# Kernel tuning notes

Hardware: AMD Instinct MI355X
Metric: run time of the kernel (lower is better)

Reference implementation:

```python
import jax, jax.numpy as jnp
import numpy as np

N = 100000   # num_nodes
E = 1600000  # num_edges
H = 128      # hidden_dim
OUT = 1      # output_dim
SLOPE = 0.2  # GATConv leaky_relu negative_slope


def setup_inputs() -> dict:
    key = jax.random.key(0)
    ks = jax.random.split(key, 10)
    s = 1.0 / np.sqrt(H)
    return {
        "h": jnp.arange(N, dtype=jnp.int64 if jax.config.jax_enable_x64 else jnp.int32),
        "edge_index": jax.random.randint(ks[0], (2, E), 0, N),
        "node_type": jax.random.randint(ks[1], (N,), 0, 3),
        "emb": jax.random.normal(ks[2], (N, H), jnp.float32) * s,
        "W1": jax.random.normal(ks[3], (H, H), jnp.float32) * s,
        "a_src1": jax.random.normal(ks[4], (H,), jnp.float32) * s,
        "a_dst1": jax.random.normal(ks[5], (H,), jnp.float32) * s,
        "b1": jnp.zeros((H,), jnp.float32),
        "W2": jax.random.normal(ks[6], (H, OUT), jnp.float32) * s,
        "a_src2": jax.random.normal(ks[7], (OUT,), jnp.float32) * s,
        "a_dst2": jax.random.normal(ks[8], (OUT,), jnp.float32) * s,
        "b2": jnp.zeros((OUT,), jnp.float32),
    }


def gat_layer(x, src, dst, emask, W, a_src, a_dst, b, n_nodes):
    """PyG GATConv (heads=1, add_self_loops=True). Masked edges get -inf logits."""
    xp = x @ W                                  # [N, F]
    e_src = xp @ a_src                          # [N]
    e_dst = xp @ a_dst                          # [N]
    logits = jax.nn.leaky_relu(e_src[src] + e_dst[dst], SLOPE)   # [E]
    logits = jnp.where(emask, logits, -jnp.inf)
    self_logits = jax.nn.leaky_relu(e_src + e_dst, SLOPE)        # [N] self-loops
    # segment softmax over destination nodes (edges + self loop)
    m = jax.ops.segment_max(logits, dst, num_segments=n_nodes)
    m = jnp.maximum(m, self_logits)             # finite: self loop always present
    ew = jnp.exp(logits - m[dst])               # masked edges -> exp(-inf)=0
    sw = jnp.exp(self_logits - m)
    denom = jax.ops.segment_sum(ew, dst, num_segments=n_nodes) + sw
    alpha = ew / denom[dst]                     # [E]
    alpha_self = sw / denom                     # [N]
    out = jax.ops.segment_sum(alpha[:, None] * xp[src], dst, num_segments=n_nodes)
    out = out + alpha_self[:, None] * xp + b
    return out


def reference(h, edge_index, node_type, emb, W1, a_src1, a_dst1, b1, W2, a_src2, a_dst2, b2):
    src, dst = edge_index[0], edge_index[1]
    emask = (node_type[src] == 0) & (node_type[dst] == 0)
    x = emb[h]                                          # embedding lookup [N, H]
    x = gat_layer(x, src, dst, emask, W1, a_src1, a_dst1, b1, emb.shape[0])
    x = jax.nn.relu(x)
    x = gat_layer(x, src, dst, emask, W2, a_src2, a_dst2, b2, emb.shape[0])
    return x
```

## Files before the change

kernel.cpp:

```cpp
#include <hip/hip_runtime.h>

#define N_NODES 100000
#define N_EDGES 1600000
#define HD 128
#define SLOPE 0.2f
#define NBLK 391
#define EBLK (N_EDGES / 256)

typedef __attribute__((ext_vector_type(8))) short bf16x8;
typedef __attribute__((ext_vector_type(4))) float f32x4;

__device__ __forceinline__ unsigned short f2bf(float f) {
    union { float f; unsigned u; } v; v.f = f;
    const unsigned u = v.u + 0x7FFFu + ((v.u >> 16) & 1u);
    return (unsigned short)(u >> 16);
}
__device__ __forceinline__ unsigned pack2(float lo, float hi) {
    return (unsigned)f2bf(lo) | ((unsigned)f2bf(hi) << 16);
}
__device__ __forceinline__ float bf2f(unsigned u16) {
    union { unsigned u; float f; } v; v.u = u16 << 16; return v.f;
}

__global__ __launch_bounds__(256) void zero_kernel(
    const int* __restrict__ nt, const float* __restrict__ W1,
    int* __restrict__ deg, int* __restrict__ fill, unsigned* __restrict__ umask,
    unsigned short* __restrict__ W1bfT)
{
    const int i = blockIdx.x * 256 + threadIdx.x;
    bool act = false;
    if (i < N_NODES) { deg[i] = 0; fill[i] = 0; act = (nt[i] == 0); }
    const unsigned long long bal = __ballot(act);
    const int lane = threadIdx.x & 63;
    if (lane == 0)       umask[i >> 5] = (unsigned)bal;
    else if (lane == 32) umask[i >> 5] = (unsigned)(bal >> 32);
    if (i < HD * HD) {
        const int n = i >> 7, k = i & 127;
        W1bfT[n * HD + k] = f2bf(W1[k * HD + n]);
    }
}

__global__ __launch_bounds__(512, 8) void gemm1_kernel(
    const int* __restrict__ h,
    const float* __restrict__ emb,
    const unsigned short* __restrict__ W1bfT,
    const float* __restrict__ a_src1,
    const float* __restrict__ a_dst1,
    unsigned short* __restrict__ xp1,
    float* __restrict__ es1,
    float* __restrict__ ed1,
    float* __restrict__ denom1)
{
    __shared__ unsigned short Wlds[HD * HD];

    const int tid = threadIdx.x;

    {
        const int n  = tid >> 2;
        const int kq = (tid & 3) * 32;
        const unsigned short* src = W1bfT + n * HD + kq;
        #pragma unroll
        for (int j = 0; j < 4; ++j) {
            const int c = (kq >> 3) + j;
            const int p = c ^ (n & 7);
            *(bf16x8*)(Wlds + n * HD + p * 8) = *(const bf16x8*)(src + j * 8);
        }
    }

    const int w   = tid >> 6;
    const int L   = tid & 63;
    const int lm  = L & 15;
    const int lg  = L >> 4;
    const int wrow0 = blockIdx.x * 128 + w * 16;

    const int arow = wrow0 + lm;
    const int g = (arow < N_NODES) ? arow : (N_NODES - 1);
    const float* xrow = emb + (size_t)h[g] * HD;

    __syncthreads();

    f32x4 acc[8];
    #pragma unroll
    for (int ct = 0; ct < 8; ++ct) acc[ct] = (f32x4)0.f;

    #pragma unroll
    for (int ks = 0; ks < 4; ++ks) {
        const int k0 = ks * 32 + lg * 8;
        const float4 u = *(const float4*)(xrow + k0);
        const float4 v = *(const float4*)(xrow + k0 + 4);
        union { bf16x8 b; unsigned x[4]; } t;
        t.x[0] = pack2(u.x, u.y);
        t.x[1] = pack2(u.z, u.w);
        t.x[2] = pack2(v.x, v.y);
        t.x[3] = pack2(v.z, v.w);
        const bf16x8 af = t.b;

        const int c = k0 >> 3;
        const int p = (c ^ (lm & 7)) * 8;
        #pragma unroll
        for (int ct = 0; ct < 8; ++ct) {
            const bf16x8 bfr = *(const bf16x8*)(Wlds + (ct * 16 + lm) * HD + p);
            acc[ct] = __builtin_amdgcn_mfma_f32_16x16x32_bf16(af, bfr, acc[ct], 0, 0, 0);
        }
    }

    float asv[8], adv[8];
    #pragma unroll
    for (int ct = 0; ct < 8; ++ct) {
        asv[ct] = a_src1[ct * 16 + lm];
        adv[ct] = a_dst1[ct * 16 + lm];
    }

    #pragma unroll
    for (int reg = 0; reg < 4; ++reg) {
        const int row = wrow0 + lg * 4 + reg;
        float s = 0.f, d = 0.f;
        #pragma unroll
        for (int ct = 0; ct < 8; ++ct) {
            s += acc[ct][reg] * asv[ct];
            d += acc[ct][reg] * adv[ct];
        }
        #pragma unroll
        for (int m = 1; m < 16; m <<= 1) {
            s += __shfl_xor(s, m, 64);
            d += __shfl_xor(d, m, 64);
        }
        if (row < N_NODES) {
            unsigned short* dst = xp1 + (size_t)row * HD;
            #pragma unroll
            for (int ct = 0; ct < 8; ++ct)
                dst[ct * 16 + lm] = f2bf(acc[ct][reg]);
            if (lm == 0) {
                const float sum = s + d;
                const float l = sum > 0.f ? sum : SLOPE * sum;
                es1[row] = s;
                ed1[row] = d;
                denom1[row] = __expf(l);
            }
        }
    }
}

__global__ __launch_bounds__(256) void edgeA_kernel(
    const int* __restrict__ ei, const unsigned* __restrict__ umask,
    const float* __restrict__ es1, const float* __restrict__ ed1,
    int* __restrict__ deg, int* __restrict__ blockCount,
    int* __restrict__ qsrc, int* __restrict__ qdst, float* __restrict__ qw)
{
    __shared__ int wcnt[4];
    const int e = blockIdx.x * 256 + threadIdx.x;
    const int wid = threadIdx.x >> 6;
    const int lane = threadIdx.x & 63;

    const int src = ei[e];
    const int dst = ei[N_EDGES + e];
    const bool active =
        (((umask[src >> 5] >> (src & 31)) & (umask[dst >> 5] >> (dst & 31))) & 1u) != 0u;

    const unsigned long long bal = __ballot(active);
    if (lane == 0) wcnt[wid] = (int)__popcll(bal);
    __syncthreads();
    const int c0w = wcnt[0], c1w = wcnt[1], c2w = wcnt[2], c3w = wcnt[3];
    if (threadIdx.x == 0) blockCount[blockIdx.x] = c0w + c1w + c2w + c3w;

    if (active) {
        int base = 0;
        if (wid > 0) base += c0w;
        if (wid > 1) base += c1w;
        if (wid > 2) base += c2w;
        atomicAdd(deg + dst, 1);
        const float logit = es1[src] + ed1[dst];
        const float l = logit > 0.f ? logit : SLOPE * logit;
        const int slot = blockIdx.x * 256 + base +
                         (int)__popcll(bal & ((1ull << lane) - 1ull));
        qsrc[slot] = src;
        qdst[slot] = dst;
        qw[slot] = __expf(l);
    }
}

__global__ __launch_bounds__(256) void bsum_kernel(
    const int* __restrict__ deg, int* __restrict__ bsum)
{
    __shared__ int wsum[4];
    const int i = blockIdx.x * 256 + threadIdx.x;
    int v = (i < N_NODES) ? deg[i] : 0;
    #pragma unroll
    for (int off = 32; off > 0; off >>= 1) v += __shfl_down(v, off, 64);
    if ((threadIdx.x & 63) == 0) wsum[threadIdx.x >> 6] = v;
    __syncthreads();
    if (threadIdx.x == 0) bsum[blockIdx.x] = wsum[0] + wsum[1] + wsum[2] + wsum[3];
}

__global__ __launch_bounds__(512) void bscan_kernel(
    const int* __restrict__ bsum, int* __restrict__ bscan, int* __restrict__ rowptr)
{
    __shared__ int s[512];
    const int t = threadIdx.x;
    const int v = (t < NBLK) ? bsum[t] : 0;
    s[t] = v;
    __syncthreads();
    #pragma unroll
    for (int off = 1; off < 512; off <<= 1) {
        const int u = (t >= off) ? s[t - off] : 0;
        __syncthreads();
        s[t] += u;
        __syncthreads();
    }
    if (t < NBLK) bscan[t] = s[t] - v;
    if (t == 0) rowptr[N_NODES] = s[NBLK - 1];
}

__global__ __launch_bounds__(256) void rowptr_kernel(
    const int* __restrict__ deg, const int* __restrict__ bscan, int* __restrict__ rowptr)
{
    __shared__ int s[256];
    const int t = threadIdx.x;
    const int i = blockIdx.x * 256 + t;
    const int v = (i < N_NODES) ? deg[i] : 0;
    s[t] = v;
    __syncthreads();
    #pragma unroll
    for (int off = 1; off < 256; off <<= 1) {
        const int u = (t >= off) ? s[t - off] : 0;
        __syncthreads();
        s[t] += u;
        __syncthreads();
    }
    if (i < N_NODES) rowptr[i] = bscan[blockIdx.x] + s[t] - v;
}

__global__ __launch_bounds__(256) void scatterB_kernel(
    const int* __restrict__ qsrc, const int* __restrict__ qdst,
    const float* __restrict__ qw, const int* __restrict__ blockCount,
    const int* __restrict__ rowptr, int* __restrict__ fill,
    int* __restrict__ esrc, float* __restrict__ ew)
{
    const int t = threadIdx.x;
    for (int b = blockIdx.x; b < EBLK; b += gridDim.x) {
        const int cnt = blockCount[b];
        if (t < cnt) {
            const int i = b * 256 + t;
            const int dst = qdst[i];
            const int slot = rowptr[dst] + atomicAdd(fill + dst, 1);
            esrc[slot] = qsrc[i];
            ew[slot] = qw[i];
        }
    }
}

__global__ __launch_bounds__(256) void gather1_kernel(
    const unsigned short* __restrict__ xp1, const float* __restrict__ denom1,
    const int* __restrict__ rowptr, const int* __restrict__ esrc,
    const float* __restrict__ ew,
    const float* __restrict__ b1, const float* __restrict__ W2,
    float* __restrict__ xp2)
{
    const int wid = threadIdx.x >> 6;
    const int lane = threadIdx.x & 63;
    const int i = blockIdx.x * 4 + wid;
    if (i >= N_NODES) return;

    const int begin = rowptr[i];
    const int end   = rowptr[i + 1];
    const float wself = denom1[i];

    const unsigned pself = ((const unsigned*)(xp1 + (size_t)i * HD))[lane];
    float a0 = wself * bf2f(pself & 0xFFFFu);
    float a1 = wself * bf2f(pself >> 16);
    float denom = wself;

    int sN = 0; float wN = 0.f;
    if (begin < end) { sN = esrc[begin]; wN = ew[begin]; }
    for (int j = begin; j < end; ++j) {
        const int s = sN; const float w = wN;
        if (j + 1 < end) { sN = esrc[j + 1]; wN = ew[j + 1]; }
        const unsigned pv = ((const unsigned*)(xp1 + (size_t)s * HD))[lane];
        a0 += w * bf2f(pv & 0xFFFFu);
        a1 += w * bf2f(pv >> 16);
        denom += w;
    }

    const float inv = 1.f / denom;
    const float o0 = fmaxf(a0 * inv + b1[2 * lane],     0.f);
    const float o1 = fmaxf(a1 * inv + b1[2 * lane + 1], 0.f);

    float part = o0 * W2[2 * lane] + o1 * W2[2 * lane + 1];
    #pragma unroll
    for (int off = 32; off > 0; off >>= 1) part += __shfl_down(part, off, 64);
    if (lane == 0) xp2[i] = part;
}

__global__ __launch_bounds__(256) void final2_kernel(
    const float* __restrict__ xp2, const int* __restrict__ rowptr,
    const int* __restrict__ esrc,
    const float* __restrict__ a_src2, const float* __restrict__ a_dst2,
    const float* __restrict__ b2, float* __restrict__ out)
{
    const int i = blockIdx.x * 256 + threadIdx.x;
    if (i >= N_NODES) return;

    const float as = a_src2[0], ad = a_dst2[0];
    const float xi = xp2[i];
    const float s0 = (as + ad) * xi;
    const float l0 = s0 > 0.f ? s0 : SLOPE * s0;
    const float wself = __expf(l0);

    float denom = wself, num = wself * xi;
    const int end = rowptr[i + 1];
    for (int j = rowptr[i]; j < end; ++j) {
        const float xsv = xp2[esrc[j]];
        const float lg = as * xsv + ad * xi;
        const float ll = lg > 0.f ? lg : SLOPE * lg;
        const float w = __expf(ll);
        denom += w;
        num += w * xsv;
    }
    out[i] = num / denom + b2[0];
}

extern "C" void kernel_launch(void* const* d_in, const int* in_sizes, int n_in,
                              void* d_out, int out_size, void* d_ws, size_t ws_size,
                              hipStream_t stream)
{
    const int* h   = (const int*)d_in[0];
    const int* ei  = (const int*)d_in[1];
    const int* nt  = (const int*)d_in[2];
    const float* emb    = (const float*)d_in[3];
    const float* W1     = (const float*)d_in[4];
    const float* a_src1 = (const float*)d_in[5];
    const float* a_dst1 = (const float*)d_in[6];
    const float* b1     = (const float*)d_in[7];
    const float* W2     = (const float*)d_in[8];
    const float* a_src2 = (const float*)d_in[9];
    const float* a_dst2 = (const float*)d_in[10];
    const float* b2     = (const float*)d_in[11];
    float* out = (float*)d_out;

    char* ws = (char*)d_ws;
    size_t off = 0;
    unsigned short* xp1 = (unsigned short*)(ws + off); off += (size_t)N_NODES * HD * sizeof(unsigned short);
    float* es1    = (float*)(ws + off); off += (size_t)N_NODES * sizeof(float);
    float* ed1    = (float*)(ws + off); off += (size_t)N_NODES * sizeof(float);
    float* denom1 = (float*)(ws + off); off += (size_t)N_NODES * sizeof(float);
    float* xp2    = (float*)(ws + off); off += (size_t)N_NODES * sizeof(float);
    int*   deg    = (int*)(ws + off);   off += (size_t)N_NODES * sizeof(int);
    int*   fill   = (int*)(ws + off);   off += (size_t)N_NODES * sizeof(int);
    int*   rowptr = (int*)(ws + off);   off += ((size_t)N_NODES + 1) * sizeof(int);
    int*   bsum   = (int*)(ws + off);   off += (size_t)NBLK * sizeof(int);
    int*   bscan  = (int*)(ws + off);   off += (size_t)NBLK * sizeof(int);
    int*   bcnt   = (int*)(ws + off);   off += (size_t)EBLK * sizeof(int);
    unsigned* umask = (unsigned*)(ws + off); off += 3200 * sizeof(unsigned);
    unsigned short* W1bfT = (unsigned short*)(ws + off); off += (size_t)HD * HD * sizeof(unsigned short);
    off = (off + 255) & ~(size_t)255;
    int*   qsrc   = (int*)(ws + off);   off += (size_t)N_EDGES * sizeof(int);
    int*   qdst   = (int*)(ws + off);   off += (size_t)N_EDGES * sizeof(int);
    float* qw     = (float*)(ws + off); off += (size_t)N_EDGES * sizeof(float);
    int*   esrc   = (int*)(ws + off);   off += (size_t)N_EDGES * sizeof(int);
    float* ew     = (float*)(ws + off); off += (size_t)N_EDGES * sizeof(float);

    zero_kernel<<<NBLK, 256, 0, stream>>>(nt, W1, deg, fill, umask, W1bfT);
    gemm1_kernel<<<(N_NODES + 127) / 128, 512, 0, stream>>>(
        h, emb, W1bfT, a_src1, a_dst1, xp1, es1, ed1, denom1);
    edgeA_kernel<<<EBLK, 256, 0, stream>>>(
        ei, umask, es1, ed1, deg, bcnt, qsrc, qdst, qw);
    bsum_kernel<<<NBLK, 256, 0, stream>>>(deg, bsum);
    bscan_kernel<<<1, 512, 0, stream>>>(bsum, bscan, rowptr);
    rowptr_kernel<<<NBLK, 256, 0, stream>>>(deg, bscan, rowptr);
    scatterB_kernel<<<512, 256, 0, stream>>>(
        qsrc, qdst, qw, bcnt, rowptr, fill, esrc, ew);
    gather1_kernel<<<(N_NODES + 3) / 4, 256, 0, stream>>>(
        xp1, denom1, rowptr, esrc, ew, b1, W2, xp2);
    final2_kernel<<<NBLK, 256, 0, stream>>>(
        xp2, rowptr, esrc, a_src2, a_dst2, b2, out);
}
```

Before: 202.5 us.

## Fuse edge filtering into GEMM launch, single-pass scan, packed int2 CSR edges

Edge filtering and degree counting now run as extra blocks inside the GEMM launch, so the edge pass can overlap with the dense work. The three-kernel prefix scan becomes one decoupled-lookback scan that uses per-block status words. The attention weight is computed during the scatter rather than stored in the queue, and the CSR source index and weight are packed into one int2 array. This cuts launches and memory traffic, at the cost of spin-waiting in the scan, which depends on blocks being scheduled in order.

New measurement: 189.9 us. 6.2% less time.

```diff
diff --git a/kernel.cpp b/kernel.cpp
--- a/kernel.cpp
+++ b/kernel.cpp
@@ -5,7 +5,9 @@
 #define HD 128
 #define SLOPE 0.2f
 #define NBLK 391
-#define EBLK (N_EDGES / 256)
+#define GB 782
+#define EB2 3125
+#define SCANB 391
 
 typedef __attribute__((ext_vector_type(8))) short bf16x8;
 typedef __attribute__((ext_vector_type(4))) float f32x4;
@@ -22,10 +24,10 @@
     union { unsigned u; float f; } v; v.u = u16 << 16; return v.f;
 }
 
-__global__ __launch_bounds__(256) void zero_kernel(
+__global__ __launch_bounds__(256) void k0_zero(
     const int* __restrict__ nt, const float* __restrict__ W1,
     int* __restrict__ deg, int* __restrict__ fill, unsigned* __restrict__ umask,
-    unsigned short* __restrict__ W1bfT)
+    unsigned short* __restrict__ W1bfT, unsigned long long* __restrict__ stat)
 {
     const int i = blockIdx.x * 256 + threadIdx.x;
     bool act = false;
@@ -38,9 +40,10 @@
         const int n = i >> 7, k = i & 127;
         W1bfT[n * HD + k] = f2bf(W1[k * HD + n]);
     }
-}
-
-__global__ __launch_bounds__(512, 8) void gemm1_kernel(
+    if (threadIdx.x == 0) stat[blockIdx.x] = 0ull;
+}
+
+__global__ __launch_bounds__(512, 8) void k1_gemm_edge(
     const int* __restrict__ h,
     const float* __restrict__ emb,
     const unsigned short* __restrict__ W1bfT,
@@ -49,11 +52,47 @@
     unsigned short* __restrict__ xp1,
     float* __restrict__ es1,
     float* __restrict__ ed1,
-    float* __restrict__ denom1)
+    float* __restrict__ denom1,
+    const int* __restrict__ ei,
+    const unsigned* __restrict__ umask,
+    int* __restrict__ deg,
+    int* __restrict__ bcnt,
+    int* __restrict__ qsrc,
+    int* __restrict__ qdst)
 {
     __shared__ unsigned short Wlds[HD * HD];
-
     const int tid = threadIdx.x;
+
+    if (blockIdx.x >= GB) {
+        int* wcnt = (int*)Wlds;
+        const int eb = blockIdx.x - GB;
+        const int e = eb * 512 + tid;
+        const int wid = tid >> 6;
+        const int lane = tid & 63;
+        const int src = ei[e];
+        const int dst = ei[N_EDGES + e];
+        const bool active =
+            (((umask[src >> 5] >> (src & 31)) & (umask[dst >> 5] >> (dst & 31))) & 1u) != 0u;
+        const unsigned long long bal = __ballot(active);
+        if (lane == 0) wcnt[wid] = (int)__popcll(bal);
+        __syncthreads();
+        int base = 0, tot = 0;
+        #pragma unroll
+        for (int k = 0; k < 8; ++k) {
+            const int c = wcnt[k];
+            if (k < wid) base += c;
+            tot += c;
+        }
+        if (tid == 0) bcnt[eb] = tot;
+        if (active) {
+            atomicAdd(deg + dst, 1);
+            const int slot = eb * 512 + base +
+                             (int)__popcll(bal & ((1ull << lane) - 1ull));
+            qsrc[slot] = src;
+            qdst[slot] = dst;
+        }
+        return;
+    }
 
     {
         const int n  = tid >> 2;
@@ -141,83 +180,29 @@
     }
 }
 
-__global__ __launch_bounds__(256) void edgeA_kernel(
-    const int* __restrict__ ei, const unsigned* __restrict__ umask,
-    const float* __restrict__ es1, const float* __restrict__ ed1,
-    int* __restrict__ deg, int* __restrict__ blockCount,
-    int* __restrict__ qsrc, int* __restrict__ qdst, float* __restrict__ qw)
-{
-    __shared__ int wcnt[4];
-    const int e = blockIdx.x * 256 + threadIdx.x;
-    const int wid = threadIdx.x >> 6;
-    const int lane = threadIdx.x & 63;
-
-    const int src = ei[e];
-    const int dst = ei[N_EDGES + e];
-    const bool active =
-        (((umask[src >> 5] >> (src & 31)) & (umask[dst >> 5] >> (dst & 31))) & 1u) != 0u;
-
-    const unsigned long long bal = __ballot(active);
-    if (lane == 0) wcnt[wid] = (int)__popcll(bal);
+__global__ __launch_bounds__(256) void k2_scan(
+    const int* __restrict__ deg,
+    unsigned long long* __restrict__ stat,
+    int* __restrict__ rowptr)
+{
+    __shared__ int s[256];
+    __shared__ int aux[6];
+    const int t = threadIdx.x;
+    const int b = blockIdx.x;
+    const int i = b * 256 + t;
+    const int v = (i < N_NODES) ? deg[i] : 0;
+
+    int r = v;
+    #pragma unroll
+    for (int m = 32; m > 0; m >>= 1) r += __shfl_down(r, m, 64);
+    if ((t & 63) == 0) aux[t >> 6] = r;
     __syncthreads();
-    const int c0w = wcnt[0], c1w = wcnt[1], c2w = wcnt[2], c3w = wcnt[3];
-    if (threadIdx.x == 0) blockCount[blockIdx.x] = c0w + c1w + c2w + c3w;
-
-    if (active) {
-        int base = 0;
-        if (wid > 0) base += c0w;
-        if (wid > 1) base += c1w;
-        if (wid > 2) base += c2w;
-        atomicAdd(deg + dst, 1);
-        const float logit = es1[src] + ed1[dst];
-        const float l = logit > 0.f ? logit : SLOPE * logit;
-        const int slot = blockIdx.x * 256 + base +
-                         (int)__popcll(bal & ((1ull << lane) - 1ull));
-        qsrc[slot] = src;
-        qdst[slot] = dst;
-        qw[slot] = __expf(l);
-    }
-}
-
-__global__ __launch_bounds__(256) void bsum_kernel(
-    const int* __restrict__ deg, int* __restrict__ bsum)
-{
-    __shared__ int wsum[4];
-    const int i = blockIdx.x * 256 + threadIdx.x;
-    int v = (i < N_NODES) ? deg[i] : 0;
-    #pragma unroll
-    for (int off = 32; off > 0; off >>= 1) v += __shfl_down(v, off, 64);
-    if ((threadIdx.x & 63) == 0) wsum[threadIdx.x >> 6] = v;
-    __syncthreads();
-    if (threadIdx.x == 0) bsum[blockIdx.x] = wsum[0] + wsum[1] + wsum[2] + wsum[3];
-}
-
-__global__ __launch_bounds__(512) void bscan_kernel(
-    const int* __restrict__ bsum, int* __restrict__ bscan, int* __restrict__ rowptr)
-{
-    __shared__ int s[512];
-    const int t = threadIdx.x;
-    const int v = (t < NBLK) ? bsum[t] : 0;
-    s[t] = v;
-    __syncthreads();
-    #pragma unroll
-    for (int off = 1; off < 512; off <<= 1) {
-        const int u = (t >= off) ? s[t - off] : 0;
-        __syncthreads();
-        s[t] += u;
-        __syncthreads();
-    }
-    if (t < NBLK) bscan[t] = s[t] - v;
-    if (t == 0) rowptr[N_NODES] = s[NBLK - 1];
-}
-
-__global__ __launch_bounds__(256) void rowptr_kernel(
-    const int* __restrict__ deg, const int* __restrict__ bscan, int* __restrict__ rowptr)
-{
-    __shared__ int s[256];
-    const int t = threadIdx.x;
-    const int i = blockIdx.x * 256 + t;
-    const int v = (i < N_NODES) ? deg[i] : 0;
+    if (t == 0) {
+        const int total = aux[0] + aux[1] + aux[2] + aux[3];
+        aux[5] = total;
+        atomicExch(stat + b, (1ull << 32) | (unsigned)total);
+    }
+
     s[t] = v;
     __syncthreads();
     #pragma unroll
@@ -227,32 +212,61 @@
         s[t] += u;
         __syncthreads();
     }
-    if (i < N_NODES) rowptr[i] = bscan[blockIdx.x] + s[t] - v;
-}
-
-__global__ __launch_bounds__(256) void scatterB_kernel(
+
+    if (t < 64) {
+        int exclusive = 0;
+        int pred = b - 1;
+        while (true) {
+            const int idx = pred - t;
+            unsigned long long e = 2ull << 32;
+            if (idx >= 0) {
+                do { e = atomicAdd(stat + idx, 0ull); } while ((e >> 32) == 0ull);
+            }
+            const unsigned long long ib = __ballot((e >> 32) >= 2ull);
+            const int fi = (int)__ffsll(ib) - 1;
+            int contrib = (fi >= 0 && t > fi) ? 0 : (int)(unsigned)e;
+            #pragma unroll
+            for (int m = 32; m > 0; m >>= 1) contrib += __shfl_down(contrib, m, 64);
+            exclusive += __shfl(contrib, 0, 64);
+            if (fi >= 0) break;
+            pred -= 64;
+        }
+        if (t == 0) {
+            const int total = aux[5];
+            atomicExch(stat + b, (2ull << 32) | (unsigned)(exclusive + total));
+            aux[4] = exclusive;
+        }
+    }
+    __syncthreads();
+    const int excl = aux[4];
+    if (i < N_NODES) rowptr[i] = excl + s[t] - v;
+    if (b == SCANB - 1 && t == 255) rowptr[N_NODES] = excl + aux[5];
+}
+
+__global__ __launch_bounds__(512) void k3_scatter(
     const int* __restrict__ qsrc, const int* __restrict__ qdst,
-    const float* __restrict__ qw, const int* __restrict__ blockCount,
+    const int* __restrict__ bcnt,
+    const float* __restrict__ es1, const float* __restrict__ ed1,
     const int* __restrict__ rowptr, int* __restrict__ fill,
-    int* __restrict__ esrc, float* __restrict__ ew)
-{
+    int2* __restrict__ ee)
+{
+    const int b = blockIdx.x;
     const int t = threadIdx.x;
-    for (int b = blockIdx.x; b < EBLK; b += gridDim.x) {
-        const int cnt = blockCount[b];
-        if (t < cnt) {
-            const int i = b * 256 + t;
-            const int dst = qdst[i];
-            const int slot = rowptr[dst] + atomicAdd(fill + dst, 1);
-            esrc[slot] = qsrc[i];
-            ew[slot] = qw[i];
-        }
-    }
-}
-
-__global__ __launch_bounds__(256) void gather1_kernel(
+    const int cnt = bcnt[b];
+    if (t < cnt) {
+        const int i = b * 512 + t;
+        const int src = qsrc[i];
+        const int dst = qdst[i];
+        const float logit = es1[src] + ed1[dst];
+        const float l = logit > 0.f ? logit : SLOPE * logit;
+        const int slot = rowptr[dst] + atomicAdd(fill + dst, 1);
+        ee[slot] = make_int2(src, __float_as_int(__expf(l)));
+    }
+}
+
+__global__ __launch_bounds__(256) void k4_gather(
     const unsigned short* __restrict__ xp1, const float* __restrict__ denom1,
-    const int* __restrict__ rowptr, const int* __restrict__ esrc,
-    const float* __restrict__ ew,
+    const int* __restrict__ rowptr, const int2* __restrict__ ee,
     const float* __restrict__ b1, const float* __restrict__ W2,
     float* __restrict__ xp2)
 {
@@ -270,11 +284,12 @@
     float a1 = wself * bf2f(pself >> 16);
     float denom = wself;
 
-    int sN = 0; float wN = 0.f;
-    if (begin < end) { sN = esrc[begin]; wN = ew[begin]; }
+    int2 nxt = make_int2(0, 0);
+    if (begin < end) nxt = ee[begin];
     for (int j = begin; j < end; ++j) {
-        const int s = sN; const float w = wN;
-        if (j + 1 < end) { sN = esrc[j + 1]; wN = ew[j + 1]; }
+        const int s = nxt.x;
+        const float w = __int_as_float(nxt.y);
+        if (j + 1 < end) nxt = ee[j + 1];
         const unsigned pv = ((const unsigned*)(xp1 + (size_t)s * HD))[lane];
         a0 += w * bf2f(pv & 0xFFFFu);
         a1 += w * bf2f(pv >> 16);
@@ -291,9 +306,9 @@
     if (lane == 0) xp2[i] = part;
 }
 
-__global__ __launch_bounds__(256) void final2_kernel(
+__global__ __launch_bounds__(256) void k5_final(
     const float* __restrict__ xp2, const int* __restrict__ rowptr,
-    const int* __restrict__ esrc,
+    const int2* __restrict__ ee,
     const float* __restrict__ a_src2, const float* __restrict__ a_dst2,
     const float* __restrict__ b2, float* __restrict__ out)
 {
@@ -309,7 +324,7 @@
     float denom = wself, num = wself * xi;
     const int end = rowptr[i + 1];
     for (int j = rowptr[i]; j < end; ++j) {
-        const float xsv = xp2[esrc[j]];
+        const float xsv = xp2[ee[j].x];
         const float lg = as * xsv + ad * xi;
         const float ll = lg > 0.f ? lg : SLOPE * lg;
         const float w = __expf(ll);
@@ -347,30 +362,25 @@
     int*   deg    = (int*)(ws + off);   off += (size_t)N_NODES * sizeof(int);
     int*   fill   = (int*)(ws + off);   off += (size_t)N_NODES * sizeof(int);
     int*   rowptr = (int*)(ws + off);   off += ((size_t)N_NODES + 1) * sizeof(int);
-    int*   bsum   = (int*)(ws + off);   off += (size_t)NBLK * sizeof(int);
-    int*   bscan  = (int*)(ws + off);   off += (size_t)NBLK * sizeof(int);
-    int*   bcnt   = (int*)(ws + off);   off += (size_t)EBLK * sizeof(int);
+    int*   bcnt   = (int*)(ws + off);   off += (size_t)EB2 * sizeof(int);
     unsigned* umask = (unsigned*)(ws + off); off += 3200 * sizeof(unsigned);
     unsigned short* W1bfT = (unsigned short*)(ws + off); off += (size_t)HD * HD * sizeof(unsigned short);
     off = (off + 255) & ~(size_t)255;
+    unsigned long long* stat = (unsigned long long*)(ws + off); off += (size_t)SCANB * sizeof(unsigned long long);
+    off = (off + 255) & ~(size_t)255;
     int*   qsrc   = (int*)(ws + off);   off += (size_t)N_EDGES * sizeof(int);
     int*   qdst   = (int*)(ws + off);   off += (size_t)N_EDGES * sizeof(int);
-    float* qw     = (float*)(ws + off); off += (size_t)N_EDGES * sizeof(float);
-    int*   esrc   = (int*)(ws + off);   off += (size_t)N_EDGES * sizeof(int);
-    float* ew     = (float*)(ws + off); off += (size_t)N_EDGES * sizeof(float);
-
-    zero_kernel<<<NBLK, 256, 0, stream>>>(nt, W1, deg, fill, umask, W1bfT);
-    gemm1_kernel<<<(N_NODES + 127) / 128, 512, 0, stream>>>(
-        h, emb, W1bfT, a_src1, a_dst1, xp1, es1, ed1, denom1);
-    edgeA_kernel<<<EBLK, 256, 0, stream>>>(
-        ei, umask, es1, ed1, deg, bcnt, qsrc, qdst, qw);
-    bsum_kernel<<<NBLK, 256, 0, stream>>>(deg, bsum);
-    bscan_kernel<<<1, 512, 0, stream>>>(bsum, bscan, rowptr);
-    rowptr_kernel<<<NBLK, 256, 0, stream>>>(deg, bscan, rowptr);
-    scatterB_kernel<<<512, 256, 0, stream>>>(
-        qsrc, qdst, qw, bcnt, rowptr, fill, esrc, ew);
-    gather1_kernel<<<(N_NODES + 3) / 4, 256, 0, stream>>>(
-        xp1, denom1, rowptr, esrc, ew, b1, W2, xp2);
-    final2_kernel<<<NBLK, 256, 0, stream>>>(
-        xp2, rowptr, esrc, a_src2, a_dst2, b2, out);
-}
+    off = (off + 255) & ~(size_t)255;
+    int2*  ee     = (int2*)(ws + off);  off += (size_t)N_EDGES * sizeof(int2);
+
+    k0_zero<<<NBLK, 256, 0, stream>>>(nt, W1, deg, fill, umask, W1bfT, stat);
+    k1_gemm_edge<<<GB + EB2, 512, 0, stream>>>(
+        h, emb, W1bfT, a_src1, a_dst1, xp1, es1, ed1, denom1,
+        ei, umask, deg, bcnt, qsrc, qdst);
+    k2_scan<<<SCANB, 256, 0, stream>>>(deg, stat, rowptr);
+    k3_scatter<<<EB2, 512, 0, stream>>>(qsrc, qdst, bcnt, es1, ed1, rowptr, fill, ee);
+    k4_gather<<<(N_NODES + 3) / 4, 256, 0, stream>>>(
+        xp1, denom1, rowptr, ee, b1, W2, xp2);
+    k5_final<<<NBLK, 256, 0, stream>>>(
+        xp2, rowptr, ee, a_src2, a_dst2, b2, out);
+}
```
